# Performance work log

Measured on AMD Instinct MI355X. Metric: run time of the kernel, lower is better.

The kernel has to match this reference:

```python
import jax, jax.numpy as jnp
import numpy as np

N_NODES = 8192
N_GRAPHS = 16
KNN_K = 80
N_FEAT = 6
KNN_COLS = (0, 1, 2, 3)
HID = 128
HID6 = 6 * HID
N_LABELS = 3
BN_EPS = 1e-5


def knn_edges(pos, batch, k):
    # pos: [N, 4]; batch: [N] graph ids. Returns (src, tgt) with k neighbors per node,
    # restricted to same graph, excluding self (PyG knn_graph, flow source_to_target).
    n = pos.shape[0]
    sq = jnp.sum(pos * pos, axis=1)
    d2 = sq[:, None] + sq[None, :] - 2.0 * (pos @ pos.T)  # [N, N]
    valid = (batch[:, None] == batch[None, :]) & ~jnp.eye(n, dtype=bool)
    d2 = jnp.where(valid, d2, jnp.inf)
    _, idx = jax.lax.top_k(-d2, k)  # k smallest distances per row
    src = idx.reshape(-1)                      # neighbor j (message source)
    tgt = jnp.repeat(jnp.arange(n), k)         # center node i (message target)
    return src, tgt


def tag_conv(x, src, tgt, norm, W, b):
    # TAGConv K=2: out = sum_k (A_hat^k x) W_k + b, A_hat = D^-1/2 A D^-1/2
    n = x.shape[0]
    out = x @ W[0]
    h = x
    for k in range(1, W.shape[0]):
        h = jax.ops.segment_sum(norm[:, None] * h[src], tgt, num_segments=n)
        out = out + h @ W[k]
    return out + b


def pool_mean_max(x, batch, n_graphs):
    cnt = jax.ops.segment_sum(jnp.ones((x.shape[0],), x.dtype), batch, num_segments=n_graphs)
    mean = jax.ops.segment_sum(x, batch, num_segments=n_graphs) / cnt[:, None]
    mx = jax.ops.segment_max(x, batch, num_segments=n_graphs)
    return jnp.concatenate([mean, mx], axis=1)


def setup_inputs() -> dict:
    key = jax.random.key(0)
    ks = jax.random.split(key, 16)
    x = jax.random.normal(ks[0], (N_NODES, N_FEAT), dtype=jnp.float32)
    batch = jnp.repeat(jnp.arange(N_GRAPHS, dtype=jnp.int32), N_NODES // N_GRAPHS)
    s1 = 1.0 / np.sqrt(N_FEAT)
    s2 = 1.0 / np.sqrt(HID)
    s3 = 1.0 / np.sqrt(HID6)
    return {
        "x": x,
        "batch": batch,
        "conv1_w": jax.random.uniform(ks[1], (3, N_FEAT, HID), jnp.float32, -s1, s1),
        "conv1_b": jnp.zeros((HID,), jnp.float32),
        "conv2_w": jax.random.uniform(ks[2], (3, HID, HID), jnp.float32, -s2, s2),
        "conv2_b": jnp.zeros((HID,), jnp.float32),
        "conv3_w": jax.random.uniform(ks[3], (3, HID, HID), jnp.float32, -s2, s2),
        "conv3_b": jnp.zeros((HID,), jnp.float32),
        "bn_gamma": jnp.ones((HID6,), jnp.float32),
        "bn_beta": jnp.zeros((HID6,), jnp.float32),
        "bn_mean": 0.1 * jax.random.normal(ks[4], (HID6,), jnp.float32),
        "bn_var": jax.random.uniform(ks[5], (HID6,), jnp.float32, 0.5, 1.5),
        "lin_w": jax.random.uniform(ks[6], (5, HID6, HID6), jnp.float32, -s3, s3),
        "lin_b": jax.random.uniform(ks[7], (5, HID6), jnp.float32, -s3, s3),
        "out_w": jax.random.uniform(ks[8], (HID6, N_LABELS), jnp.float32, -s3, s3),
        "out_b": jax.random.uniform(ks[9], (N_LABELS,), jnp.float32, -s3, s3),
    }


def reference(x, batch, conv1_w, conv1_b, conv2_w, conv2_b, conv3_w, conv3_b,
              bn_gamma, bn_beta, bn_mean, bn_var, lin_w, lin_b, out_w, out_b):
    n = x.shape[0]
    pos = x[:, jnp.array(KNN_COLS)]
    src, tgt = knn_edges(pos, batch, KNN_K)
    # gcn_norm without self loops (edge dropout disabled: eval-mode determinism)
    deg = jax.ops.segment_sum(jnp.ones_like(src, dtype=x.dtype), tgt, num_segments=n)
    dinv = jnp.where(deg > 0, jax.lax.rsqrt(jnp.maximum(deg, 1.0)), 0.0)
    norm = dinv[src] * dinv[tgt]

    h = jax.nn.leaky_relu(tag_conv(x, src, tgt, norm, conv1_w, conv1_b))
    p1 = pool_mean_max(h, batch, N_GRAPHS)
    h = jax.nn.leaky_relu(tag_conv(h, src, tgt, norm, conv2_w, conv2_b))
    p2 = pool_mean_max(h, batch, N_GRAPHS)
    h = jax.nn.leaky_relu(tag_conv(h, src, tgt, norm, conv3_w, conv3_b))
    p3 = pool_mean_max(h, batch, N_GRAPHS)

    g = jnp.concatenate([p1, p2, p3], axis=1)  # [B, 768]
    g = (g - bn_mean) * jax.lax.rsqrt(bn_var + BN_EPS) * bn_gamma + bn_beta
    for i in range(lin_w.shape[0]):
        g = jax.nn.leaky_relu(g @ lin_w[i] + lin_b[i])
    out = g @ out_w + out_b
    return out.reshape(-1, N_LABELS)
```

## Files before the change

kernel.cpp:

```cpp
#include <hip/hip_runtime.h>

constexpr int N    = 8192;
constexpr int NPG  = 512;
constexpr int NG   = 16;
constexpr int KNN  = 80;
constexpr int F0   = 6;
constexpr int HID  = 128;
constexpr int H6   = 768;
constexpr int RPB  = 16;
constexpr int BPGR = NPG / RPB;

__device__ __forceinline__ float leaky(float v) { return v > 0.0f ? v : 0.01f * v; }

__device__ __forceinline__ int lanes_below(unsigned long long m) {
    return __builtin_amdgcn_mbcnt_hi((unsigned)(m >> 32),
           __builtin_amdgcn_mbcnt_lo((unsigned)m, 0));
}

__device__ __forceinline__ int wave_count_sum(int c) {
    int total = 0;
    #pragma unroll
    for (int b = 0; b < 4; b++)
        total += (int)__popcll(__ballot((c >> b) & 1)) << b;
    return total;
}

__global__ __launch_bounds__(256) void knn_kernel(const float* __restrict__ x,
                                                  int* __restrict__ nbr) {
    constexpr int BPG = 128;
    const int tid  = threadIdx.x;
    const int lane = tid & 63;
    const int wv   = tid >> 6;
    const int base = (blockIdx.x / BPG) << 9;
    const int t    = base + (blockIdx.x & (BPG - 1)) * 4 + wv;
    const int tl   = t - base;

    __shared__ float px[512], py[512], pz[512], pw[512];
    __shared__ unsigned long long skey[4 * 128];

    for (int j = tid; j < 512; j += 256) {
        const float* row = x + (size_t)(base + j) * F0;
        const float2 ra = *(const float2*)(row);
        const float2 rb = *(const float2*)(row + 2);
        px[j] = ra.x; py[j] = ra.y; pz[j] = rb.x; pw[j] = rb.y;
    }
    __syncthreads();

    const float tx = px[tl], ty = py[tl], tz = pz[tl], tw = pw[tl];
    const float sqt = tx*tx + ty*ty + tz*tz + tw*tw;

    unsigned d2m[8];
    #pragma unroll
    for (int j = 0; j < 8; j++) {
        const int node = j * 64 + lane;
        const float jx = px[node], jy = py[node], jz = pz[node], jw = pw[node];
        const float sqj = jx*jx + jy*jy + jz*jz + jw*jw;
        const float dot = tx*jx + ty*jy + tz*jz + tw*jw;
        const float d2  = sqt + sqj - 2.0f * dot;
        unsigned u = __float_as_uint(d2);
        u = (u & 0x80000000u) ? ~u : (u | 0x80000000u);
        d2m[j] = (node == tl) ? 0xFFFFFFFFu : u;
    }

    unsigned V = 0;
    for (int b = 31; b >= 0; --b) {
        const unsigned test = V | (1u << b);
        int c = 0;
        #pragma unroll
        for (int j = 0; j < 8; j++) c += (d2m[j] < test) ? 1 : 0;
        if (wave_count_sum(c) < KNN) V = test;
    }

    int c = 0;
    #pragma unroll
    for (int j = 0; j < 8; j++) c += (d2m[j] < V) ? 1 : 0;
    const int n_lt = wave_count_sum(c);
    const int need = KNN - n_lt;

    const int woff = wv * 128;
    int cnt_total = 0, taken = 0;
    #pragma unroll
    for (int j = 0; j < 8; j++) {
        const bool lt = d2m[j] < V;
        const bool eq = d2m[j] == V;
        const unsigned long long meq = __ballot(eq);
        const bool sel = lt || (eq && (taken + lanes_below(meq)) < need);
        taken += (int)__popcll(meq);
        const unsigned long long msel = __ballot(sel);
        if (sel) {
            const int pos = cnt_total + lanes_below(msel);
            skey[woff + pos] = ((unsigned long long)d2m[j] << 32)
                             | (unsigned)(base + j * 64 + lane);
        }
        cnt_total += (int)__popcll(msel);
    }
    for (int i = KNN + lane; i < 128; i += 64) skey[woff + i] = ~0ULL;
    __syncthreads();

    for (int kk = 2; kk <= 128; kk <<= 1) {
        for (int jj = kk >> 1; jj >= 1; jj >>= 1) {
            const int i  = ((lane & ~(jj - 1)) << 1) | (lane & (jj - 1));
            const int ix = i | jj;
            const unsigned long long a = skey[woff + i];
            const unsigned long long b = skey[woff + ix];
            const bool up = ((i & kk) == 0);
            if ((a > b) == up) { skey[woff + i] = b; skey[woff + ix] = a; }
            __syncthreads();
        }
    }

    if (lane < KNN)      nbr[t * KNN + lane]      = (int)(unsigned)skey[woff + lane];
    if (lane + 64 < KNN) nbr[t * KNN + lane + 64] = (int)(unsigned)skey[woff + lane + 64];
}

__global__ __launch_bounds__(256) void prop6(const float* __restrict__ hin,
                                             const int* __restrict__ nbr,
                                             float* __restrict__ hout) {
    const int gid = blockIdx.x * 256 + threadIdx.x;
    const int t   = gid >> 3;
    const int sl  = gid & 7;
    const int* nb = nbr + t * KNN + sl * 10;

    float a[F0] = {0.f, 0.f, 0.f, 0.f, 0.f, 0.f};
    #pragma unroll
    for (int j = 0; j < 10; j++) {
        const float* r = hin + (size_t)nb[j] * F0;
        #pragma unroll
        for (int f = 0; f < F0; f++) a[f] += r[f];
    }
    #pragma unroll
    for (int off = 1; off < 8; off <<= 1)
        #pragma unroll
        for (int f = 0; f < F0; f++) a[f] += __shfl_xor(a[f], off);

    if (sl == 0) {
        const float inv = 1.0f / 80.0f;
        float* o = hout + (size_t)t * F0;
        #pragma unroll
        for (int f = 0; f < F0; f++) o[f] = a[f] * inv;
    }
}

__global__ __launch_bounds__(256) void prop128(const float* __restrict__ hin,
                                               const int* __restrict__ nbr,
                                               float* __restrict__ hout) {
    const int lane = threadIdx.x & 31;
    const int t    = blockIdx.x * 8 + (threadIdx.x >> 5);
    const int* nb  = nbr + t * KNN;
    float a0=0.f,a1=0.f,a2=0.f,a3=0.f;
    for (int i = 0; i < KNN; i += 16) {
        const int4 sA = *(const int4*)(nb + i);
        const int4 sB = *(const int4*)(nb + i + 4);
        const int4 sC = *(const int4*)(nb + i + 8);
        const int4 sD = *(const int4*)(nb + i + 12);
        const int idx[16] = {sA.x,sA.y,sA.z,sA.w, sB.x,sB.y,sB.z,sB.w,
                             sC.x,sC.y,sC.z,sC.w, sD.x,sD.y,sD.z,sD.w};
        float4 v[16];
        #pragma unroll
        for (int q = 0; q < 16; q++)
            v[q] = *(const float4*)(hin + (size_t)idx[q] * HID + lane * 4);
        #pragma unroll
        for (int q = 0; q < 16; q += 4) {
            a0 += (v[q].x + v[q+1].x) + (v[q+2].x + v[q+3].x);
            a1 += (v[q].y + v[q+1].y) + (v[q+2].y + v[q+3].y);
            a2 += (v[q].z + v[q+1].z) + (v[q+2].z + v[q+3].z);
            a3 += (v[q].w + v[q+1].w) + (v[q+2].w + v[q+3].w);
        }
    }
    const float inv = 1.0f / 80.0f;
    float4 r; r.x=a0*inv; r.y=a1*inv; r.z=a2*inv; r.w=a3*inv;
    *(float4*)(hout + (size_t)t * HID + lane * 4) = r;
}

template<int K>
__global__ __launch_bounds__(256) void combine_kernel(const float* __restrict__ X,
                                                      const float* __restrict__ Y1,
                                                      const float* __restrict__ Y2,
                                                      const float* __restrict__ W,
                                                      const float* __restrict__ bias,
                                                      float* __restrict__ out,
                                                      float* __restrict__ psum,
                                                      float* __restrict__ pmax) {
    __shared__ float xs[3][RPB * K];
    const int tid  = threadIdx.x;
    const int row0 = blockIdx.x * RPB;

    {
        const float* s0 = X  + (size_t)row0 * K;
        const float* s1 = Y1 + (size_t)row0 * K;
        const float* s2 = Y2 + (size_t)row0 * K;
        if constexpr ((K & 3) == 0) {
            constexpr int NV = RPB * K / 4;
            for (int i = tid; i < NV; i += 256) ((float4*)xs[0])[i] = ((const float4*)s0)[i];
            for (int i = tid; i < NV; i += 256) ((float4*)xs[1])[i] = ((const float4*)s1)[i];
            for (int i = tid; i < NV; i += 256) ((float4*)xs[2])[i] = ((const float4*)s2)[i];
        } else {
            for (int i = tid; i < RPB * K; i += 256) xs[0][i] = s0[i];
            for (int i = tid; i < RPB * K; i += 256) xs[1][i] = s1[i];
            for (int i = tid; i < RPB * K; i += 256) xs[2][i] = s2[i];
        }
    }
    __syncthreads();

    const int c  = tid & 127;
    const int r0 = (tid >> 7) * 8;

    float acc[8];
    #pragma unroll
    for (int r = 0; r < 8; r++) acc[r] = 0.0f;

    #pragma unroll
    for (int s = 0; s < 3; s++) {
        const float* __restrict__ Ws   = W + (size_t)s * K * HID;
        const float* __restrict__ xseg = xs[s] + r0 * K;
        for (int k = 0; k < K; k += 2) {
            const float w0 = Ws[(size_t)k * HID + c];
            const float w1 = Ws[(size_t)(k + 1) * HID + c];
            #pragma unroll
            for (int r = 0; r < 8; r++)
                acc[r] += xseg[r * K + k] * w0 + xseg[r * K + k + 1] * w1;
        }
    }

    const float bb = bias[c];
    float sum8 = 0.0f, mx8 = -3.402823e38f;
    #pragma unroll
    for (int r = 0; r < 8; r++) {
        const float v = leaky(acc[r] + bb);
        out[(size_t)(row0 + r0 + r) * HID + c] = v;
        sum8 += v;
        mx8 = fmaxf(mx8, v);
    }

    __shared__ float ssum[128], smx[128];
    if (r0) { ssum[c] = sum8; smx[c] = mx8; }
    __syncthreads();
    if (!r0) {
        psum[(size_t)blockIdx.x * HID + c] = sum8 + ssum[c];
        pmax[(size_t)blockIdx.x * HID + c] = fmaxf(mx8, smx[c]);
    }
}

__global__ __launch_bounds__(256) void lin0_kernel(const float* __restrict__ psum1,
                                                   const float* __restrict__ pmax1,
                                                   const float* __restrict__ psum2,
                                                   const float* __restrict__ pmax2,
                                                   const float* __restrict__ psum3,
                                                   const float* __restrict__ pmax3,
                                                   const float* __restrict__ gamma,
                                                   const float* __restrict__ beta,
                                                   const float* __restrict__ mean,
                                                   const float* __restrict__ var,
                                                   const float* __restrict__ W,
                                                   const float* __restrict__ bias,
                                                   float* __restrict__ gout) {
    const int r   = blockIdx.x / 6;
    const int cc  = blockIdx.x % 6;
    const int tid = threadIdx.x;

    __shared__ float gs[H6];
    {
        const int cv = tid >> 7;
        const int c  = tid & 127;
        const float* ps = (cv ? psum2 : psum1) + (size_t)r * BPGR * HID + c;
        const float* pm = (cv ? pmax2 : pmax1) + (size_t)r * BPGR * HID + c;
        float s = 0.0f, m = -3.402823e38f;
        #pragma unroll 8
        for (int b = 0; b < BPGR; b++) { s += ps[b * HID]; m = fmaxf(m, pm[b * HID]); }
        gs[cv * 256 + c]       = s * (1.0f / 512.0f);
        gs[cv * 256 + 128 + c] = m;
    }
    if (tid < 128) {
        const float* ps = psum3 + (size_t)r * BPGR * HID + tid;
        const float* pm = pmax3 + (size_t)r * BPGR * HID + tid;
        float s = 0.0f, m = -3.402823e38f;
        #pragma unroll 8
        for (int b = 0; b < BPGR; b++) { s += ps[b * HID]; m = fmaxf(m, pm[b * HID]); }
        gs[512 + tid]       = s * (1.0f / 512.0f);
        gs[512 + 128 + tid] = m;
    }
    __syncthreads();
    for (int k = tid; k < H6; k += 256)
        gs[k] = (gs[k] - mean[k]) * (1.0f / sqrtf(var[k] + 1e-5f)) * gamma[k] + beta[k];
    __syncthreads();

    const int c  = cc * 128 + (tid & 127);
    const int kh = tid >> 7;
    const int kb = kh * 384;
    float a0=0.f,a1=0.f,a2=0.f,a3=0.f;
    for (int k = kb; k < kb + 384; k += 4) {
        a0 += gs[k]     * W[(size_t)(k)     * H6 + c];
        a1 += gs[k + 1] * W[(size_t)(k + 1) * H6 + c];
        a2 += gs[k + 2] * W[(size_t)(k + 2) * H6 + c];
        a3 += gs[k + 3] * W[(size_t)(k + 3) * H6 + c];
    }
    __shared__ float part[256];
    part[tid] = (a0 + a1) + (a2 + a3);
    __syncthreads();
    if (kh == 0) {
        const float v = part[tid] + part[tid + 128] + bias[c];
        gout[(size_t)r * H6 + c] = leaky(v);
    }
}

__global__ __launch_bounds__(256) void lin_kernel(const float* __restrict__ gin,
                                                  const float* __restrict__ W,
                                                  const float* __restrict__ bias,
                                                  float* __restrict__ gout) {
    const int r   = blockIdx.x / 6;
    const int cc  = blockIdx.x % 6;
    const int tid = threadIdx.x;

    __shared__ float gs[H6];
    for (int k = tid; k < H6; k += 256) gs[k] = gin[(size_t)r * H6 + k];
    __syncthreads();

    const int c  = cc * 128 + (tid & 127);
    const int kh = tid >> 7;
    const int kb = kh * 384;
    float a0=0.f,a1=0.f,a2=0.f,a3=0.f;
    for (int k = kb; k < kb + 384; k += 4) {
        a0 += gs[k]     * W[(size_t)(k)     * H6 + c];
        a1 += gs[k + 1] * W[(size_t)(k + 1) * H6 + c];
        a2 += gs[k + 2] * W[(size_t)(k + 2) * H6 + c];
        a3 += gs[k + 3] * W[(size_t)(k + 3) * H6 + c];
    }
    __shared__ float part[256];
    part[tid] = (a0 + a1) + (a2 + a3);
    __syncthreads();
    if (kh == 0) {
        const float v = part[tid] + part[tid + 128] + bias[c];
        gout[(size_t)r * H6 + c] = leaky(v);
    }
}

__global__ void out_kernel(const float* __restrict__ gin,
                           const float* __restrict__ W,
                           const float* __restrict__ bias,
                           float* __restrict__ out) {
    const int tid = threadIdx.x;
    __shared__ float part[192];
    if (tid < 192) {
        const int q  = tid >> 2;
        const int r  = q / 3, c = q % 3;
        const int kq = tid & 3;
        float acc = 0.0f;
        for (int k = kq * 192; k < kq * 192 + 192; k++)
            acc += gin[(size_t)r * H6 + k] * W[(size_t)k * 3 + c];
        part[tid] = acc;
    }
    __syncthreads();
    if (tid < 48) {
        const int r = tid / 3, c = tid % 3;
        out[r * 3 + c] = part[tid*4] + part[tid*4+1] + part[tid*4+2] + part[tid*4+3] + bias[c];
    }
}

extern "C" void kernel_launch(void* const* d_in, const int* in_sizes, int n_in,
                              void* d_out, int out_size, void* d_ws, size_t ws_size,
                              hipStream_t stream) {
    const float* x        = (const float*)d_in[0];
    const float* conv1_w  = (const float*)d_in[2];
    const float* conv1_b  = (const float*)d_in[3];
    const float* conv2_w  = (const float*)d_in[4];
    const float* conv2_b  = (const float*)d_in[5];
    const float* conv3_w  = (const float*)d_in[6];
    const float* conv3_b  = (const float*)d_in[7];
    const float* bn_gamma = (const float*)d_in[8];
    const float* bn_beta  = (const float*)d_in[9];
    const float* bn_mean  = (const float*)d_in[10];
    const float* bn_var   = (const float*)d_in[11];
    const float* lin_w    = (const float*)d_in[12];
    const float* lin_b    = (const float*)d_in[13];
    const float* out_w    = (const float*)d_in[14];
    const float* out_b    = (const float*)d_in[15];

    char* ws = (char*)d_ws;
    size_t off = 0;
    auto alloc = [&](size_t bytes) {
        void* p = ws + off;
        off += (bytes + 255) & ~(size_t)255;
        return p;
    };
    int*   nbr   = (int*)  alloc((size_t)N * KNN * 4);
    float* y6a   = (float*)alloc((size_t)N * F0 * 4);
    float* y6b   = (float*)alloc((size_t)N * F0 * 4);
    float* hA    = (float*)alloc((size_t)N * HID * 4);
    float* hB    = (float*)alloc((size_t)N * HID * 4);
    float* y1    = (float*)alloc((size_t)N * HID * 4);
    float* y2    = (float*)alloc((size_t)N * HID * 4);
    float* ga    = (float*)alloc((size_t)NG * H6 * 4);
    float* gb    = (float*)alloc((size_t)NG * H6 * 4);
    float* psum1 = (float*)alloc((size_t)(N / RPB) * HID * 4);
    float* pmax1 = (float*)alloc((size_t)(N / RPB) * HID * 4);
    float* psum2 = (float*)alloc((size_t)(N / RPB) * HID * 4);
    float* pmax2 = (float*)alloc((size_t)(N / RPB) * HID * 4);
    float* psum3 = (float*)alloc((size_t)(N / RPB) * HID * 4);
    float* pmax3 = (float*)alloc((size_t)(N / RPB) * HID * 4);

    knn_kernel<<<N / 4, 256, 0, stream>>>(x, nbr);

    prop6<<<N * 8 / 256, 256, 0, stream>>>(x, nbr, y6a);
    prop6<<<N * 8 / 256, 256, 0, stream>>>(y6a, nbr, y6b);
    combine_kernel<6><<<N / RPB, 256, 0, stream>>>(x, y6a, y6b, conv1_w, conv1_b, hA, psum1, pmax1);

    prop128<<<N / 8, 256, 0, stream>>>(hA, nbr, y1);
    prop128<<<N / 8, 256, 0, stream>>>(y1, nbr, y2);
    combine_kernel<128><<<N / RPB, 256, 0, stream>>>(hA, y1, y2, conv2_w, conv2_b, hB, psum2, pmax2);

    prop128<<<N / 8, 256, 0, stream>>>(hB, nbr, y1);
    prop128<<<N / 8, 256, 0, stream>>>(y1, nbr, y2);
    combine_kernel<128><<<N / RPB, 256, 0, stream>>>(hB, y1, y2, conv3_w, conv3_b, hA, psum3, pmax3);

    lin0_kernel<<<96, 256, 0, stream>>>(psum1, pmax1, psum2, pmax2, psum3, pmax3,
                                        bn_gamma, bn_beta, bn_mean, bn_var,
                                        lin_w + 0 * H6 * H6, lin_b + 0 * H6, gb);
    lin_kernel<<<96, 256, 0, stream>>>(gb, lin_w + 1 * H6 * H6, lin_b + 1 * H6, ga);
    lin_kernel<<<96, 256, 0, stream>>>(ga, lin_w + 2 * H6 * H6, lin_b + 2 * H6, gb);
    lin_kernel<<<96, 256, 0, stream>>>(gb, lin_w + 3 * H6 * H6, lin_b + 3 * H6, ga);
    lin_kernel<<<96, 256, 0, stream>>>(ga, lin_w + 4 * H6 * H6, lin_b + 4 * H6, gb);
    out_kernel<<<1, 256, 0, stream>>>(gb, out_w, out_b, (float*)d_out);
}
```

Measured before the change: 265.5 us.

## Fuse two-hop propagation into LDS-resident per-graph kernel and fuse MLP head

Each two-hop 128-wide propagation now runs as one kernel. A block stages a whole graph's 512 nodes for a 4-column slice into LDS and computes both hops there, so the second hop no longer gathers y1 from global memory. The five linear layers and the output layer become a single per-graph head kernel, cutting five launches. The risk is that the head now runs on only 16 blocks, each streaming all five 768x768 weight matrices with less parallelism. The propagation also relies on neighbors staying inside the same graph (the index & 511 mask) and re-reads the neighbor lists once per column slice.

```diff
diff --git a/kernel.cpp b/kernel.cpp
--- a/kernel.cpp
+++ b/kernel.cpp
@@ -141,35 +141,75 @@
     }
 }
 
-__global__ __launch_bounds__(256) void prop128(const float* __restrict__ hin,
-                                               const int* __restrict__ nbr,
-                                               float* __restrict__ hout) {
-    const int lane = threadIdx.x & 31;
-    const int t    = blockIdx.x * 8 + (threadIdx.x >> 5);
-    const int* nb  = nbr + t * KNN;
-    float a0=0.f,a1=0.f,a2=0.f,a3=0.f;
-    for (int i = 0; i < KNN; i += 16) {
-        const int4 sA = *(const int4*)(nb + i);
-        const int4 sB = *(const int4*)(nb + i + 4);
-        const int4 sC = *(const int4*)(nb + i + 8);
-        const int4 sD = *(const int4*)(nb + i + 12);
-        const int idx[16] = {sA.x,sA.y,sA.z,sA.w, sB.x,sB.y,sB.z,sB.w,
-                             sC.x,sC.y,sC.z,sC.w, sD.x,sD.y,sD.z,sD.w};
-        float4 v[16];
-        #pragma unroll
-        for (int q = 0; q < 16; q++)
-            v[q] = *(const float4*)(hin + (size_t)idx[q] * HID + lane * 4);
-        #pragma unroll
-        for (int q = 0; q < 16; q += 4) {
-            a0 += (v[q].x + v[q+1].x) + (v[q+2].x + v[q+3].x);
-            a1 += (v[q].y + v[q+1].y) + (v[q+2].y + v[q+3].y);
-            a2 += (v[q].z + v[q+1].z) + (v[q+2].z + v[q+3].z);
-            a3 += (v[q].w + v[q+1].w) + (v[q+2].w + v[q+3].w);
-        }
-    }
+__global__ __launch_bounds__(256) void prop2x(const float* __restrict__ H,
+                                              const int* __restrict__ nbr,
+                                              float* __restrict__ y1,
+                                              float* __restrict__ y2) {
+    constexpr int PCW = 4;
+    __shared__ float b0[512 * PCW];
+    __shared__ float b1[512 * PCW];
+    const int g    = blockIdx.x >> 5;
+    const int cc   = blockIdx.x & 31;
+    const int c0   = cc * PCW;
+    const int tid  = threadIdx.x;
+    const int base = g << 9;
     const float inv = 1.0f / 80.0f;
-    float4 r; r.x=a0*inv; r.y=a1*inv; r.z=a2*inv; r.w=a3*inv;
-    *(float4*)(hout + (size_t)t * HID + lane * 4) = r;
+
+    for (int r = tid; r < 512; r += 256)
+        *(float4*)&b0[r * PCW] = *(const float4*)(H + (size_t)(base + r) * HID + c0);
+    __syncthreads();
+
+    #pragma unroll
+    for (int rr = 0; rr < 2; rr++) {
+        const int r = tid + rr * 256;
+        const int* nb = nbr + (size_t)(base + r) * KNN;
+        float a0=0.f,a1=0.f,a2=0.f,a3=0.f;
+        for (int i = 0; i < KNN; i += 8) {
+            const int4 qa = *(const int4*)(nb + i);
+            const int4 qb = *(const int4*)(nb + i + 4);
+            const float4 v0 = *(const float4*)&b0[(qa.x & 511) * PCW];
+            const float4 v1 = *(const float4*)&b0[(qa.y & 511) * PCW];
+            const float4 v2 = *(const float4*)&b0[(qa.z & 511) * PCW];
+            const float4 v3 = *(const float4*)&b0[(qa.w & 511) * PCW];
+            const float4 v4 = *(const float4*)&b0[(qb.x & 511) * PCW];
+            const float4 v5 = *(const float4*)&b0[(qb.y & 511) * PCW];
+            const float4 v6 = *(const float4*)&b0[(qb.z & 511) * PCW];
+            const float4 v7 = *(const float4*)&b0[(qb.w & 511) * PCW];
+            a0 += (v0.x+v1.x)+(v2.x+v3.x)+(v4.x+v5.x)+(v6.x+v7.x);
+            a1 += (v0.y+v1.y)+(v2.y+v3.y)+(v4.y+v5.y)+(v6.y+v7.y);
+            a2 += (v0.z+v1.z)+(v2.z+v3.z)+(v4.z+v5.z)+(v6.z+v7.z);
+            a3 += (v0.w+v1.w)+(v2.w+v3.w)+(v4.w+v5.w)+(v6.w+v7.w);
+        }
+        float4 o; o.x=a0*inv; o.y=a1*inv; o.z=a2*inv; o.w=a3*inv;
+        *(float4*)&b1[r * PCW] = o;
+        *(float4*)(y1 + (size_t)(base + r) * HID + c0) = o;
+    }
+    __syncthreads();
+
+    #pragma unroll
+    for (int rr = 0; rr < 2; rr++) {
+        const int r = tid + rr * 256;
+        const int* nb = nbr + (size_t)(base + r) * KNN;
+        float a0=0.f,a1=0.f,a2=0.f,a3=0.f;
+        for (int i = 0; i < KNN; i += 8) {
+            const int4 qa = *(const int4*)(nb + i);
+            const int4 qb = *(const int4*)(nb + i + 4);
+            const float4 v0 = *(const float4*)&b1[(qa.x & 511) * PCW];
+            const float4 v1 = *(const float4*)&b1[(qa.y & 511) * PCW];
+            const float4 v2 = *(const float4*)&b1[(qa.z & 511) * PCW];
+            const float4 v3 = *(const float4*)&b1[(qa.w & 511) * PCW];
+            const float4 v4 = *(const float4*)&b1[(qb.x & 511) * PCW];
+            const float4 v5 = *(const float4*)&b1[(qb.y & 511) * PCW];
+            const float4 v6 = *(const float4*)&b1[(qb.z & 511) * PCW];
+            const float4 v7 = *(const float4*)&b1[(qb.w & 511) * PCW];
+            a0 += (v0.x+v1.x)+(v2.x+v3.x)+(v4.x+v5.x)+(v6.x+v7.x);
+            a1 += (v0.y+v1.y)+(v2.y+v3.y)+(v4.y+v5.y)+(v6.y+v7.y);
+            a2 += (v0.z+v1.z)+(v2.z+v3.z)+(v4.z+v5.z)+(v6.z+v7.z);
+            a3 += (v0.w+v1.w)+(v2.w+v3.w)+(v4.w+v5.w)+(v6.w+v7.w);
+        }
+        float4 o; o.x=a0*inv; o.y=a1*inv; o.z=a2*inv; o.w=a3*inv;
+        *(float4*)(y2 + (size_t)(base + r) * HID + c0) = o;
+    }
 }
 
 template<int K>
@@ -241,7 +281,7 @@
     }
 }
 
-__global__ __launch_bounds__(256) void lin0_kernel(const float* __restrict__ psum1,
+__global__ __launch_bounds__(256) void head_kernel(const float* __restrict__ psum1,
                                                    const float* __restrict__ pmax1,
                                                    const float* __restrict__ psum2,
                                                    const float* __restrict__ pmax2,
@@ -251,109 +291,70 @@
                                                    const float* __restrict__ beta,
                                                    const float* __restrict__ mean,
                                                    const float* __restrict__ var,
-                                                   const float* __restrict__ W,
-                                                   const float* __restrict__ bias,
-                                                   float* __restrict__ gout) {
-    const int r   = blockIdx.x / 6;
-    const int cc  = blockIdx.x % 6;
+                                                   const float* __restrict__ lin_w,
+                                                   const float* __restrict__ lin_b,
+                                                   const float* __restrict__ out_w,
+                                                   const float* __restrict__ out_b,
+                                                   float* __restrict__ out) {
+    const int r   = blockIdx.x;
     const int tid = threadIdx.x;
-
-    __shared__ float gs[H6];
-    {
-        const int cv = tid >> 7;
-        const int c  = tid & 127;
-        const float* ps = (cv ? psum2 : psum1) + (size_t)r * BPGR * HID + c;
-        const float* pm = (cv ? pmax2 : pmax1) + (size_t)r * BPGR * HID + c;
+    __shared__ float gs[H6], gt[H6], red[H6];
+
+    for (int idx = tid; idx < 384; idx += 256) {
+        const int cv = idx >> 7, c = idx & 127;
+        const float* ps = (cv == 0 ? psum1 : cv == 1 ? psum2 : psum3)
+                        + (size_t)r * BPGR * HID + c;
+        const float* pm = (cv == 0 ? pmax1 : cv == 1 ? pmax2 : pmax3)
+                        + (size_t)r * BPGR * HID + c;
         float s = 0.0f, m = -3.402823e38f;
         #pragma unroll 8
         for (int b = 0; b < BPGR; b++) { s += ps[b * HID]; m = fmaxf(m, pm[b * HID]); }
         gs[cv * 256 + c]       = s * (1.0f / 512.0f);
         gs[cv * 256 + 128 + c] = m;
     }
-    if (tid < 128) {
-        const float* ps = psum3 + (size_t)r * BPGR * HID + tid;
-        const float* pm = pmax3 + (size_t)r * BPGR * HID + tid;
-        float s = 0.0f, m = -3.402823e38f;
-        #pragma unroll 8
-        for (int b = 0; b < BPGR; b++) { s += ps[b * HID]; m = fmaxf(m, pm[b * HID]); }
-        gs[512 + tid]       = s * (1.0f / 512.0f);
-        gs[512 + 128 + tid] = m;
-    }
     __syncthreads();
     for (int k = tid; k < H6; k += 256)
         gs[k] = (gs[k] - mean[k]) * (1.0f / sqrtf(var[k] + 1e-5f)) * gamma[k] + beta[k];
     __syncthreads();
 
-    const int c  = cc * 128 + (tid & 127);
-    const int kh = tid >> 7;
-    const int kb = kh * 384;
-    float a0=0.f,a1=0.f,a2=0.f,a3=0.f;
-    for (int k = kb; k < kb + 384; k += 4) {
-        a0 += gs[k]     * W[(size_t)(k)     * H6 + c];
-        a1 += gs[k + 1] * W[(size_t)(k + 1) * H6 + c];
-        a2 += gs[k + 2] * W[(size_t)(k + 2) * H6 + c];
-        a3 += gs[k + 3] * W[(size_t)(k + 3) * H6 + c];
-    }
-    __shared__ float part[256];
-    part[tid] = (a0 + a1) + (a2 + a3);
-    __syncthreads();
-    if (kh == 0) {
-        const float v = part[tid] + part[tid + 128] + bias[c];
-        gout[(size_t)r * H6 + c] = leaky(v);
-    }
-}
-
-__global__ __launch_bounds__(256) void lin_kernel(const float* __restrict__ gin,
-                                                  const float* __restrict__ W,
-                                                  const float* __restrict__ bias,
-                                                  float* __restrict__ gout) {
-    const int r   = blockIdx.x / 6;
-    const int cc  = blockIdx.x % 6;
-    const int tid = threadIdx.x;
-
-    __shared__ float gs[H6];
-    for (int k = tid; k < H6; k += 256) gs[k] = gin[(size_t)r * H6 + k];
-    __syncthreads();
-
-    const int c  = cc * 128 + (tid & 127);
-    const int kh = tid >> 7;
-    const int kb = kh * 384;
-    float a0=0.f,a1=0.f,a2=0.f,a3=0.f;
-    for (int k = kb; k < kb + 384; k += 4) {
-        a0 += gs[k]     * W[(size_t)(k)     * H6 + c];
-        a1 += gs[k + 1] * W[(size_t)(k + 1) * H6 + c];
-        a2 += gs[k + 2] * W[(size_t)(k + 2) * H6 + c];
-        a3 += gs[k + 3] * W[(size_t)(k + 3) * H6 + c];
-    }
-    __shared__ float part[256];
-    part[tid] = (a0 + a1) + (a2 + a3);
-    __syncthreads();
-    if (kh == 0) {
-        const float v = part[tid] + part[tid + 128] + bias[c];
-        gout[(size_t)r * H6 + c] = leaky(v);
-    }
-}
-
-__global__ void out_kernel(const float* __restrict__ gin,
-                           const float* __restrict__ W,
-                           const float* __restrict__ bias,
-                           float* __restrict__ out) {
-    const int tid = threadIdx.x;
-    __shared__ float part[192];
-    if (tid < 192) {
-        const int q  = tid >> 2;
-        const int r  = q / 3, c = q % 3;
-        const int kq = tid & 3;
-        float acc = 0.0f;
-        for (int k = kq * 192; k < kq * 192 + 192; k++)
-            acc += gin[(size_t)r * H6 + k] * W[(size_t)k * 3 + c];
-        part[tid] = acc;
-    }
-    __syncthreads();
-    if (tid < 48) {
-        const int r = tid / 3, c = tid % 3;
-        out[r * 3 + c] = part[tid*4] + part[tid*4+1] + part[tid*4+2] + part[tid*4+3] + bias[c];
-    }
+    float* src = gs;
+    float* dst = gt;
+    for (int l = 0; l < 5; l++) {
+        const float* __restrict__ W  = lin_w + (size_t)l * H6 * H6;
+        const float* __restrict__ bb = lin_b + (size_t)l * H6;
+        float a0 = 0.f, a1 = 0.f, a2 = 0.f;
+        #pragma unroll 4
+        for (int k = 0; k < H6; k++) {
+            const float g = src[k];
+            const float* wr = W + (size_t)k * H6 + tid;
+            a0 += g * wr[0];
+            a1 += g * wr[256];
+            a2 += g * wr[512];
+        }
+        dst[tid]       = leaky(a0 + bb[tid]);
+        dst[tid + 256] = leaky(a1 + bb[tid + 256]);
+        dst[tid + 512] = leaky(a2 + bb[tid + 512]);
+        __syncthreads();
+        float* tmp = src; src = dst; dst = tmp;
+    }
+
+    float a[3] = {0.f, 0.f, 0.f};
+    for (int k = tid; k < H6; k += 256) {
+        const float g = src[k];
+        a[0] += g * out_w[k * 3 + 0];
+        a[1] += g * out_w[k * 3 + 1];
+        a[2] += g * out_w[k * 3 + 2];
+    }
+    #pragma unroll
+    for (int c = 0; c < 3; c++) red[c * 256 + tid] = a[c];
+    __syncthreads();
+    for (int off = 128; off > 0; off >>= 1) {
+        if (tid < off)
+            #pragma unroll
+            for (int c = 0; c < 3; c++) red[c * 256 + tid] += red[c * 256 + tid + off];
+        __syncthreads();
+    }
+    if (tid < 3) out[r * 3 + tid] = red[tid * 256] + out_b[tid];
 }
 
 extern "C" void kernel_launch(void* const* d_in, const int* in_sizes, int n_in,
@@ -389,8 +390,6 @@
     float* hB    = (float*)alloc((size_t)N * HID * 4);
     float* y1    = (float*)alloc((size_t)N * HID * 4);
     float* y2    = (float*)alloc((size_t)N * HID * 4);
-    float* ga    = (float*)alloc((size_t)NG * H6 * 4);
-    float* gb    = (float*)alloc((size_t)NG * H6 * 4);
     float* psum1 = (float*)alloc((size_t)(N / RPB) * HID * 4);
     float* pmax1 = (float*)alloc((size_t)(N / RPB) * HID * 4);
     float* psum2 = (float*)alloc((size_t)(N / RPB) * HID * 4);
@@ -404,20 +403,13 @@
     prop6<<<N * 8 / 256, 256, 0, stream>>>(y6a, nbr, y6b);
     combine_kernel<6><<<N / RPB, 256, 0, stream>>>(x, y6a, y6b, conv1_w, conv1_b, hA, psum1, pmax1);
 
-    prop128<<<N / 8, 256, 0, stream>>>(hA, nbr, y1);
-    prop128<<<N / 8, 256, 0, stream>>>(y1, nbr, y2);
+    prop2x<<<NG * 32, 256, 0, stream>>>(hA, nbr, y1, y2);
     combine_kernel<128><<<N / RPB, 256, 0, stream>>>(hA, y1, y2, conv2_w, conv2_b, hB, psum2, pmax2);
 
-    prop128<<<N / 8, 256, 0, stream>>>(hB, nbr, y1);
-    prop128<<<N / 8, 256, 0, stream>>>(y1, nbr, y2);
+    prop2x<<<NG * 32, 256, 0, stream>>>(hB, nbr, y1, y2);
     combine_kernel<128><<<N / RPB, 256, 0, stream>>>(hB, y1, y2, conv3_w, conv3_b, hA, psum3, pmax3);
 
-    lin0_kernel<<<96, 256, 0, stream>>>(psum1, pmax1, psum2, pmax2, psum3, pmax3,
+    head_kernel<<<NG, 256, 0, stream>>>(psum1, pmax1, psum2, pmax2, psum3, pmax3,
                                         bn_gamma, bn_beta, bn_mean, bn_var,
-                                        lin_w + 0 * H6 * H6, lin_b + 0 * H6, gb);
-    lin_kernel<<<96, 256, 0, stream>>>(gb, lin_w + 1 * H6 * H6, lin_b + 1 * H6, ga);
-    lin_kernel<<<96, 256, 0, stream>>>(ga, lin_w + 2 * H6 * H6, lin_b + 2 * H6, gb);
-    lin_kernel<<<96, 256, 0, stream>>>(gb, lin_w + 3 * H6 * H6, lin_b + 3 * H6, ga);
-    lin_kernel<<<96, 256, 0, stream>>>(ga, lin_w + 4 * H6 * H6, lin_b + 4 * H6, gb);
-    out_kernel<<<1, 256, 0, stream>>>(gb, out_w, out_b, (float*)d_out);
-}
+                                        lin_w, lin_b, out_w, out_b, (float*)d_out);
+}
```

After: 535.6 us, median of 2. 2.02x slower.

## Fuse two propagation hops into one kernel with per-graph LDS column slabs

Applied to the files above, without the earlier changes.

Replaces the two prop128 launches with a single prop2x kernel. Each block stages one graph's 512 rows times four feature columns in shared memory and gathers neighbours from LDS instead of global memory. It then runs the second hop from the LDS copy of the first hop's result. This removes one launch and the global round trip of y1 between hops. The cost is that every block re-reads the full neighbour list (512x80 ints) for its column slice, 32 times per graph, and the code relies on neighbours lying in the same 512-node graph (the idx & 511 masking).

```diff
diff --git a/kernel.cpp b/kernel.cpp
--- a/kernel.cpp
+++ b/kernel.cpp
@@ -141,35 +141,75 @@
     }
 }
 
-__global__ __launch_bounds__(256) void prop128(const float* __restrict__ hin,
-                                               const int* __restrict__ nbr,
-                                               float* __restrict__ hout) {
-    const int lane = threadIdx.x & 31;
-    const int t    = blockIdx.x * 8 + (threadIdx.x >> 5);
-    const int* nb  = nbr + t * KNN;
-    float a0=0.f,a1=0.f,a2=0.f,a3=0.f;
-    for (int i = 0; i < KNN; i += 16) {
-        const int4 sA = *(const int4*)(nb + i);
-        const int4 sB = *(const int4*)(nb + i + 4);
-        const int4 sC = *(const int4*)(nb + i + 8);
-        const int4 sD = *(const int4*)(nb + i + 12);
-        const int idx[16] = {sA.x,sA.y,sA.z,sA.w, sB.x,sB.y,sB.z,sB.w,
-                             sC.x,sC.y,sC.z,sC.w, sD.x,sD.y,sD.z,sD.w};
-        float4 v[16];
-        #pragma unroll
-        for (int q = 0; q < 16; q++)
-            v[q] = *(const float4*)(hin + (size_t)idx[q] * HID + lane * 4);
-        #pragma unroll
-        for (int q = 0; q < 16; q += 4) {
-            a0 += (v[q].x + v[q+1].x) + (v[q+2].x + v[q+3].x);
-            a1 += (v[q].y + v[q+1].y) + (v[q+2].y + v[q+3].y);
-            a2 += (v[q].z + v[q+1].z) + (v[q+2].z + v[q+3].z);
-            a3 += (v[q].w + v[q+1].w) + (v[q+2].w + v[q+3].w);
-        }
-    }
+__global__ __launch_bounds__(256) void prop2x(const float* __restrict__ H,
+                                              const int* __restrict__ nbr,
+                                              float* __restrict__ y1,
+                                              float* __restrict__ y2) {
+    constexpr int PCW = 4;
+    __shared__ float b0[512 * PCW];
+    __shared__ float b1[512 * PCW];
+    const int g    = blockIdx.x >> 5;
+    const int cc   = blockIdx.x & 31;
+    const int c0   = cc * PCW;
+    const int tid  = threadIdx.x;
+    const int base = g << 9;
     const float inv = 1.0f / 80.0f;
-    float4 r; r.x=a0*inv; r.y=a1*inv; r.z=a2*inv; r.w=a3*inv;
-    *(float4*)(hout + (size_t)t * HID + lane * 4) = r;
+
+    for (int r = tid; r < 512; r += 256)
+        *(float4*)&b0[r * PCW] = *(const float4*)(H + (size_t)(base + r) * HID + c0);
+    __syncthreads();
+
+    #pragma unroll
+    for (int rr = 0; rr < 2; rr++) {
+        const int r = tid + rr * 256;
+        const int* nb = nbr + (size_t)(base + r) * KNN;
+        float a0=0.f,a1=0.f,a2=0.f,a3=0.f;
+        for (int i = 0; i < KNN; i += 8) {
+            const int4 qa = *(const int4*)(nb + i);
+            const int4 qb = *(const int4*)(nb + i + 4);
+            const float4 v0 = *(const float4*)&b0[(qa.x & 511) * PCW];
+            const float4 v1 = *(const float4*)&b0[(qa.y & 511) * PCW];
+            const float4 v2 = *(const float4*)&b0[(qa.z & 511) * PCW];
+            const float4 v3 = *(const float4*)&b0[(qa.w & 511) * PCW];
+            const float4 v4 = *(const float4*)&b0[(qb.x & 511) * PCW];
+            const float4 v5 = *(const float4*)&b0[(qb.y & 511) * PCW];
+            const float4 v6 = *(const float4*)&b0[(qb.z & 511) * PCW];
+            const float4 v7 = *(const float4*)&b0[(qb.w & 511) * PCW];
+            a0 += (v0.x+v1.x)+(v2.x+v3.x)+(v4.x+v5.x)+(v6.x+v7.x);
+            a1 += (v0.y+v1.y)+(v2.y+v3.y)+(v4.y+v5.y)+(v6.y+v7.y);
+            a2 += (v0.z+v1.z)+(v2.z+v3.z)+(v4.z+v5.z)+(v6.z+v7.z);
+            a3 += (v0.w+v1.w)+(v2.w+v3.w)+(v4.w+v5.w)+(v6.w+v7.w);
+        }
+        float4 o; o.x=a0*inv; o.y=a1*inv; o.z=a2*inv; o.w=a3*inv;
+        *(float4*)&b1[r * PCW] = o;
+        *(float4*)(y1 + (size_t)(base + r) * HID + c0) = o;
+    }
+    __syncthreads();
+
+    #pragma unroll
+    for (int rr = 0; rr < 2; rr++) {
+        const int r = tid + rr * 256;
+        const int* nb = nbr + (size_t)(base + r) * KNN;
+        float a0=0.f,a1=0.f,a2=0.f,a3=0.f;
+        for (int i = 0; i < KNN; i += 8) {
+            const int4 qa = *(const int4*)(nb + i);
+            const int4 qb = *(const int4*)(nb + i + 4);
+            const float4 v0 = *(const float4*)&b1[(qa.x & 511) * PCW];
+            const float4 v1 = *(const float4*)&b1[(qa.y & 511) * PCW];
+            const float4 v2 = *(const float4*)&b1[(qa.z & 511) * PCW];
+            const float4 v3 = *(const float4*)&b1[(qa.w & 511) * PCW];
+            const float4 v4 = *(const float4*)&b1[(qb.x & 511) * PCW];
+            const float4 v5 = *(const float4*)&b1[(qb.y & 511) * PCW];
+            const float4 v6 = *(const float4*)&b1[(qb.z & 511) * PCW];
+            const float4 v7 = *(const float4*)&b1[(qb.w & 511) * PCW];
+            a0 += (v0.x+v1.x)+(v2.x+v3.x)+(v4.x+v5.x)+(v6.x+v7.x);
+            a1 += (v0.y+v1.y)+(v2.y+v3.y)+(v4.y+v5.y)+(v6.y+v7.y);
+            a2 += (v0.z+v1.z)+(v2.z+v3.z)+(v4.z+v5.z)+(v6.z+v7.z);
+            a3 += (v0.w+v1.w)+(v2.w+v3.w)+(v4.w+v5.w)+(v6.w+v7.w);
+        }
+        float4 o; o.x=a0*inv; o.y=a1*inv; o.z=a2*inv; o.w=a3*inv;
+        *(float4*)(y2 + (size_t)(base + r) * HID + c0) = o;
+    }
 }
 
 template<int K>
@@ -404,12 +444,10 @@
     prop6<<<N * 8 / 256, 256, 0, stream>>>(y6a, nbr, y6b);
     combine_kernel<6><<<N / RPB, 256, 0, stream>>>(x, y6a, y6b, conv1_w, conv1_b, hA, psum1, pmax1);
 
-    prop128<<<N / 8, 256, 0, stream>>>(hA, nbr, y1);
-    prop128<<<N / 8, 256, 0, stream>>>(y1, nbr, y2);
+    prop2x<<<NG * 32, 256, 0, stream>>>(hA, nbr, y1, y2);
     combine_kernel<128><<<N / RPB, 256, 0, stream>>>(hA, y1, y2, conv2_w, conv2_b, hB, psum2, pmax2);
 
-    prop128<<<N / 8, 256, 0, stream>>>(hB, nbr, y1);
-    prop128<<<N / 8, 256, 0, stream>>>(y1, nbr, y2);
+    prop2x<<<NG * 32, 256, 0, stream>>>(hB, nbr, y1, y2);
     combine_kernel<128><<<N / RPB, 256, 0, stream>>>(hB, y1, y2, conv3_w, conv3_b, hA, psum3, pmax3);
 
     lin0_kernel<<<96, 256, 0, stream>>>(psum1, pmax1, psum2, pmax2, psum3, pmax3,
```

New measurement: 286.8 us. +8.0%, slower.
